# Kernel tuning notes

Measured on AMD Instinct MI355X. Metric: run time of the kernel, lower is better.

Reference implementation:

```python
import jax, jax.numpy as jnp
import numpy as np

N, L, H, D, NCLS = 8192, 1024, 512, 256, 2


def setup_inputs() -> dict:
    key = jax.random.key(0)
    ks = jax.random.split(key, 11)
    s = 0.02  # xavier-ish init scale
    return {
        "x": jax.random.normal(ks[0], (N, L), jnp.float32),
        "W_fc": jax.random.normal(ks[1], (L, H), jnp.float32) * s,
        "b_fc": jnp.zeros((H,), jnp.float32),
        "W_a": jax.random.normal(ks[2], (H, D), jnp.float32) * s,
        "b_a": jnp.zeros((D,), jnp.float32),
        "W_b": jax.random.normal(ks[3], (H, D), jnp.float32) * s,
        "b_b": jnp.zeros((D,), jnp.float32),
        "W_c": jax.random.normal(ks[4], (D, 1), jnp.float32) * s,
        "b_c": jnp.zeros((1,), jnp.float32),
        "W_cls": jax.random.normal(ks[5], (H, NCLS), jnp.float32) * s,
        "b_cls": jnp.zeros((NCLS,), jnp.float32),
    }


def reference(x, W_fc, b_fc, W_a, b_a, W_b, b_b, W_c, b_c, W_cls, b_cls):
    n = x.shape[0]
    # fc: Linear + ReLU (dropout p=0, eval)
    h = jax.nn.relu(x @ W_fc + b_fc)                      # [N, 512]
    # gated attention net (Attn_Net_Gated, n_classes=1)
    a = jnp.tanh(h @ W_a + b_a)                           # [N, 256]
    b = jax.nn.sigmoid(h @ W_b + b_b)                     # [N, 256]
    scores = ((a * b) @ W_c + b_c)[:, 0]                  # [N] diagonal scores
    # A_raw: the original's wasteful CxNxN diagonal matrix (C=1)
    idx = jnp.arange(n)
    A_raw = jnp.zeros((1, n, n), x.dtype).at[0, idx, idx].set(scores)
    # bag_forward: softmax over all N*N entries (N^2 - N zeros off-diagonal),
    # then M = (A @ h).sum(dim=1). Closed form, numerically stable:
    m = jnp.maximum(jnp.max(scores), jnp.zeros((), x.dtype))
    e = jnp.exp(scores - m)                               # diag exp terms
    e0 = jnp.exp(-m)                                      # off-diag exp(0 - m)
    Z = jnp.sum(e) + (n * n - n) * e0
    s = e / Z                                             # softmaxed diagonal
    # row_i @ h = s_i*h_i + (1/Z)*sum_{j!=i} h_j ; sum over i:
    M = s @ h + ((n - 1) * e0 / Z) * jnp.sum(h, axis=0)   # [512]
    logits = M @ W_cls + b_cls                            # [2]
    return (logits[None, :], A_raw)
```

## Files before the change

### kernel.cpp

```cpp
#include <hip/hip_runtime.h>
#include <stdint.h>

#define NROWS 8192
#define LDIM  1024
#define HDIM  512

typedef __attribute__((ext_vector_type(8))) short short8;
typedef __attribute__((ext_vector_type(4))) float f32x4;
typedef __attribute__((ext_vector_type(4))) unsigned int u32x4;

typedef __attribute__((address_space(3))) unsigned int lds_uint;
typedef const __attribute__((address_space(1))) unsigned int glob_uint;

#define Z_K1_START 0L
#define ZB_K1      3968
#define Z_G1_START 8126464L
#define ZB_G1      2560
#define Z_G2_START 13369344L
#define ZB_G2      1408
#define Z_RW_START 16252928L
#define ZB_RW      256
#define Z_END      16777215L

__device__ __forceinline__ void llds16(const void* g, void* l) {
  __builtin_amdgcn_global_load_lds((glob_uint*)g, (lds_uint*)l, 16, 0, 0);
}

__device__ __forceinline__ unsigned short f2bf(float f) {
  union { float f; unsigned int u; } c; c.f = f;
  unsigned int u = c.u;
  unsigned int r = (u + 0x7fffu + ((u >> 16) & 1u)) >> 16;
  return (unsigned short)r;
}

__device__ __forceinline__ unsigned int pkbf(float a, float b) {
  union { float f; unsigned int u; } ca, cb; ca.f = a; cb.f = b;
  return ((ca.u + 0x8000u) >> 16) | ((cb.u + 0x8000u) & 0xffff0000u);
}

__device__ __forceinline__ float bfbits2f(unsigned int hi16) {
  union { unsigned int u; float f; } c; c.u = hi16;
  return c.f;
}

__device__ __forceinline__ void zero_duty(float* __restrict__ out, long zstart, int zblk, int tid) {
  u32x4* out16 = (u32x4*)(out + 4);
  long c0 = zstart + (long)zblk * 2048;
  long c1 = c0 + 2048 < Z_END ? c0 + 2048 : Z_END;
  u32x4 z = {0u, 0u, 0u, 0u};
  for (long i = c0 + tid; i < c1; i += 256) out16[i] = z;
}

__global__ __launch_bounds__(256) void prep_kernel(const float* __restrict__ Wfc,
                                                   const float* __restrict__ Wa,
                                                   const float* __restrict__ Wb,
                                                   unsigned short* __restrict__ WfcT,
                                                   unsigned short* __restrict__ WabT,
                                                   float* __restrict__ out) {
  __shared__ float tile[32][33];
  const int bid = blockIdx.x;
  const int tid = threadIdx.x;
  if (bid < ZB_K1) {
    zero_duty(out, Z_K1_START, bid, tid);
    if (bid == 0 && tid == 0) {
      out[2] = 0.f; out[3] = 0.f;
      out[67108864] = 0.f; out[67108865] = 0.f;
    }
    return;
  }
  int tt = bid - ZB_K1;
  const float* src; unsigned short* dst; int srcn, dstk, k0, n0, mode;
  if (tt < 512) {
    src = Wfc; dst = WfcT; srcn = 512; dstk = 1024; mode = 0;
    k0 = (tt >> 4) * 32; n0 = (tt & 15) * 32;
  } else if (tt < 640) {
    int t2 = tt - 512;
    src = Wa; dst = WabT; srcn = 256; dstk = 512; mode = 1;
    k0 = (t2 >> 3) * 32; n0 = (t2 & 7) * 32;
  } else {
    int t2 = tt - 640;
    src = Wb; dst = WabT; srcn = 256; dstk = 512; mode = 2;
    k0 = (t2 >> 3) * 32; n0 = (t2 & 7) * 32;
  }
  int r = tid >> 3, c4 = (tid & 7) * 4;
  float4 v = *(const float4*)(src + (long)(k0 + r) * srcn + n0 + c4);
  tile[r][c4 + 0] = v.x; tile[r][c4 + 1] = v.y; tile[r][c4 + 2] = v.z; tile[r][c4 + 3] = v.w;
  __syncthreads();
  union { unsigned short s[4]; uint2 u; } o;
#pragma unroll
  for (int j = 0; j < 4; ++j) o.s[j] = f2bf(tile[c4 + j][r]);
  int n = n0 + r;
  long crow = (mode == 0) ? (long)n
                          : (long)(((n >> 4) << 5) + (n & 15) + (mode == 2 ? 16 : 0));
  *(uint2*)(dst + crow * dstk + k0 + c4) = o.u;
}

__global__ __launch_bounds__(256) void gemm1_kernel(const float* __restrict__ X,
                                                    const unsigned short* __restrict__ Bt,
                                                    const float* __restrict__ bias,
                                                    unsigned short* __restrict__ out,
                                                    float* __restrict__ zout) {
  constexpr int K = LDIM, nk = K / 32;
  __shared__ float sA[2][64 * 32];
  __shared__ unsigned short sB[2][128 * 32];
  const int tid = threadIdx.x;
  if ((int)blockIdx.x >= 512) {
    zero_duty(zout, Z_G1_START, (int)blockIdx.x - 512, tid);
    return;
  }
  const int lane = tid & 63;
  const int wv = tid >> 6;
  const int wm = wv >> 1, wn = wv & 1;
  const int bm = blockIdx.x >> 2, bn = blockIdx.x & 3;
  const int row0 = bm * 64, col0 = bn * 128;

  f32x4 acc[2][4] = {};

  auto stage = [&](int buf, int kt) {
#pragma unroll
    for (int r = 0; r < 2; ++r) {
      int c = r * 256 + tid;
      int ar = c >> 3, as = (c & 7) ^ (ar & 7);
      llds16(X + (long)(row0 + ar) * K + kt * 32 + as * 4,
             (float*)&sA[buf][(r * 256 + wv * 64) * 4]);
      int br = c >> 2, bs = (c & 3) ^ ((br >> 1) & 3);
      llds16(Bt + (long)(col0 + br) * K + kt * 32 + bs * 8,
             (unsigned short*)&sB[buf][(r * 256 + wv * 64) * 8]);
    }
  };

  stage(0, 0);
  __syncthreads();

  for (int kt = 0; kt < nk; ++kt) {
    int cur = kt & 1;
    if (kt + 1 < nk) stage(cur ^ 1, kt + 1);
    const float* bA = sA[cur];
    const unsigned short* bB = sB[cur];
    short8 af[2], bfr[4];
#pragma unroll
    for (int fm = 0; fm < 2; ++fm) {
      int r = wm * 32 + fm * 16 + (lane & 15);
      int g = r & 7;
      int s0 = (lane >> 4) * 2;
      float4 f0 = *(const float4*)&bA[r * 32 + ((s0)     ^ g) * 4];
      float4 f1 = *(const float4*)&bA[r * 32 + ((s0 + 1) ^ g) * 4];
      union { unsigned int u[4]; short8 s8; } o;
      o.u[0] = pkbf(f0.x, f0.y); o.u[1] = pkbf(f0.z, f0.w);
      o.u[2] = pkbf(f1.x, f1.y); o.u[3] = pkbf(f1.z, f1.w);
      af[fm] = o.s8;
    }
#pragma unroll
    for (int fn = 0; fn < 4; ++fn) {
      int rb = wn * 64 + fn * 16 + (lane & 15);
      int sb = (lane >> 4) ^ ((rb >> 1) & 3);
      bfr[fn] = *(const short8*)&bB[rb * 32 + sb * 8];
    }
#pragma unroll
    for (int fm = 0; fm < 2; ++fm)
#pragma unroll
      for (int fn = 0; fn < 4; ++fn)
        acc[fm][fn] = __builtin_amdgcn_mfma_f32_16x16x32_bf16(af[fm], bfr[fn], acc[fm][fn], 0, 0, 0);
    __syncthreads();
  }

  const float* bias_ = bias;
#pragma unroll
  for (int fm = 0; fm < 2; ++fm)
#pragma unroll
    for (int fn = 0; fn < 4; ++fn)
#pragma unroll
      for (int i = 0; i < 4; ++i) {
        int row = row0 + wm * 32 + fm * 16 + (lane >> 4) * 4 + i;
        int col = col0 + wn * 64 + fn * 16 + (lane & 15);
        float v = acc[fm][fn][i] + bias_[col];
        v = v > 0.f ? v : 0.f;
        out[(long)row * HDIM + col] = f2bf(v);
      }
}

__global__ __launch_bounds__(256) void gemm2_kernel(const unsigned short* __restrict__ A,
                                                    const unsigned short* __restrict__ Bt,
                                                    const float* __restrict__ ba_,
                                                    const float* __restrict__ bb_,
                                                    const float* __restrict__ Wc_,
                                                    float* __restrict__ spart,
                                                    float* __restrict__ zout) {
  constexpr int K = HDIM, nk = K / 32;
  __shared__ unsigned short sA[2][64 * 32];
  __shared__ unsigned short sB[2][128 * 32];
  const int tid = threadIdx.x;
  if ((int)blockIdx.x >= 512) {
    zero_duty(zout, Z_G2_START, (int)blockIdx.x - 512, tid);
    return;
  }
  const int lane = tid & 63;
  const int wv = tid >> 6;
  const int wm = wv >> 1, wn = wv & 1;
  const int bm = blockIdx.x >> 2, bn = blockIdx.x & 3;
  const int row0 = bm * 64, col0 = bn * 128;

  f32x4 acc[2][4] = {};

  auto stage = [&](int buf, int kt) {
    {
      int ar = tid >> 2, as = (tid & 3) ^ ((ar >> 1) & 3);
      llds16(A + (long)(row0 + ar) * K + kt * 32 + as * 8,
             (unsigned short*)&sA[buf][(wv * 64) * 8]);
    }
#pragma unroll
    for (int r = 0; r < 2; ++r) {
      int c = r * 256 + tid;
      int br = c >> 2, bs = (c & 3) ^ ((br >> 1) & 3);
      llds16(Bt + (long)(col0 + br) * K + kt * 32 + bs * 8,
             (unsigned short*)&sB[buf][(r * 256 + wv * 64) * 8]);
    }
  };

  stage(0, 0);
  __syncthreads();

  for (int kt = 0; kt < nk; ++kt) {
    int cur = kt & 1;
    if (kt + 1 < nk) stage(cur ^ 1, kt + 1);
    const unsigned short* bA = sA[cur];
    const unsigned short* bB = sB[cur];
    short8 af[2], bfr[4];
#pragma unroll
    for (int fm = 0; fm < 2; ++fm) {
      int r = wm * 32 + fm * 16 + (lane & 15);
      int s = (lane >> 4) ^ ((r >> 1) & 3);
      af[fm] = *(const short8*)&bA[r * 32 + s * 8];
    }
#pragma unroll
    for (int fn = 0; fn < 4; ++fn) {
      int rb = wn * 64 + fn * 16 + (lane & 15);
      int sb = (lane >> 4) ^ ((rb >> 1) & 3);
      bfr[fn] = *(const short8*)&bB[rb * 32 + sb * 8];
    }
#pragma unroll
    for (int fm = 0; fm < 2; ++fm)
#pragma unroll
      for (int fn = 0; fn < 4; ++fn)
        acc[fm][fn] = __builtin_amdgcn_mfma_f32_16x16x32_bf16(af[fm], bfr[fn], acc[fm][fn], 0, 0, 0);
    __syncthreads();
  }

#pragma unroll
  for (int g = 0; g < 2; ++g) {
    const int colg = col0 + wn * 64 + g * 32;
    const int d0 = (colg >> 5) * 16 + (lane & 15);
    float wc = Wc_[d0], av = ba_[d0], bv = bb_[d0];
    float* sp = spart + (long)(colg >> 5) * NROWS;
#pragma unroll
    for (int fm = 0; fm < 2; ++fm)
#pragma unroll
      for (int i = 0; i < 4; ++i) {
        float aa = acc[fm][g * 2 + 0][i] + av;
        float bbv = acc[fm][g * 2 + 1][i] + bv;
        float v = tanhf(aa) * (1.f / (1.f + __expf(-bbv))) * wc;
#pragma unroll
        for (int off = 1; off < 16; off <<= 1) v += __shfl_xor(v, off);
        if ((lane & 15) == 0)
          sp[row0 + wm * 32 + fm * 16 + (lane >> 4) * 4 + i] = v;
      }
  }
}

__global__ __launch_bounds__(256) void redwsum_kernel(const float* __restrict__ spart,
                                                      const float* __restrict__ bc,
                                                      const unsigned short* __restrict__ h,
                                                      float* __restrict__ part,
                                                      float* __restrict__ out) {
  const int b = blockIdx.x;
  const int t = threadIdx.x;
  if (b >= 64) {
    zero_duty(out, Z_RW_START, b - 64, t);
    return;
  }
  __shared__ float sc[NROWS];
  __shared__ float red[256];
  __shared__ float warr[128];
  const float bcv = bc[0];
  float lmax = -1e30f;
  for (int k = t; k < NROWS; k += 256) {
    float s = bcv;
#pragma unroll
    for (int q = 0; q < 16; ++q) s += spart[q * NROWS + k];
    sc[k] = s;
    lmax = fmaxf(lmax, s);
  }
  red[t] = lmax; __syncthreads();
  for (int s = 128; s; s >>= 1) { if (t < s) red[t] = fmaxf(red[t], red[t + s]); __syncthreads(); }
  float m = fmaxf(red[0], 0.f);
  __syncthreads();
  float lsum = 0.f;
  for (int k = t; k < NROWS; k += 256) lsum += __expf(sc[k] - m);
  red[t] = lsum; __syncthreads();
  for (int s = 128; s; s >>= 1) { if (t < s) red[t] += red[t + s]; __syncthreads(); }
  float e0 = __expf(-m);
  float Z = red[0] + 67100672.0f * e0;
  float c0w = 8191.0f * e0 / Z;
  if (t < 128) warr[t] = __expf(sc[b * 128 + t] - m) / Z + c0w;
  __syncthreads();
  float a0 = 0.f, a1 = 0.f;
  for (int i = 0; i < 128; ++i) {
    float wi = warr[i];
    unsigned int hv = *(const unsigned int*)&h[(long)(b * 128 + i) * 512 + t * 2];
    a0 += wi * bfbits2f(hv << 16);
    a1 += wi * bfbits2f(hv & 0xffff0000u);
  }
  part[b * 512 + t * 2] = a0;
  part[b * 512 + t * 2 + 1] = a1;
}

__global__ __launch_bounds__(512) void final_kernel(const float* __restrict__ part,
                                                    const float* __restrict__ spart,
                                                    const float* __restrict__ bc,
                                                    const float* __restrict__ Wcls,
                                                    const float* __restrict__ bcls,
                                                    float* __restrict__ out) {
  const int t = threadIdx.x;
  if (blockIdx.x > 0) {
    if (t < 256) {
      int row = (blockIdx.x - 1) * 256 + t;
      float s = bc[0];
#pragma unroll
      for (int q = 0; q < 16; ++q) s += spart[q * NROWS + row];
      out[2 + 8193L * row] = s;
    }
    return;
  }
  __shared__ float Msh[512];
  float s = 0.f;
  for (int b = 0; b < 64; ++b) s += part[b * 512 + t];
  Msh[t] = s;
  __syncthreads();
  if (t < 64) {
    float p0 = 0.f, p1 = 0.f;
    for (int j = t; j < 512; j += 64) { p0 += Msh[j] * Wcls[j * 2]; p1 += Msh[j] * Wcls[j * 2 + 1]; }
#pragma unroll
    for (int off = 32; off; off >>= 1) { p0 += __shfl_down(p0, off); p1 += __shfl_down(p1, off); }
    if (t == 0) { out[0] = p0 + bcls[0]; out[1] = p1 + bcls[1]; }
  }
}

extern "C" void kernel_launch(void* const* d_in, const int* in_sizes, int n_in,
                              void* d_out, int out_size, void* d_ws, size_t ws_size,
                              hipStream_t stream) {
  const float* x    = (const float*)d_in[0];
  const float* Wfc  = (const float*)d_in[1];
  const float* bfc  = (const float*)d_in[2];
  const float* Wa   = (const float*)d_in[3];
  const float* ba   = (const float*)d_in[4];
  const float* Wb   = (const float*)d_in[5];
  const float* bb   = (const float*)d_in[6];
  const float* Wc   = (const float*)d_in[7];
  const float* bc   = (const float*)d_in[8];
  const float* Wcls = (const float*)d_in[9];
  const float* bcls = (const float*)d_in[10];
  float* out = (float*)d_out;
  char* ws = (char*)d_ws;

  unsigned short* WfcT  = (unsigned short*)(ws + 0);
  unsigned short* WabT  = (unsigned short*)(ws + 1048576);
  unsigned short* hbuf  = (unsigned short*)(ws + 1572864);
  float*          spart = (float*)(ws + 9961472);
  float*          part  = (float*)(ws + 10485760);

  prep_kernel<<<ZB_K1 + 768, 256, 0, stream>>>(Wfc, Wa, Wb, WfcT, WabT, out);
  gemm1_kernel<<<512 + ZB_G1, 256, 0, stream>>>(x, WfcT, bfc, hbuf, out);
  gemm2_kernel<<<512 + ZB_G2, 256, 0, stream>>>(hbuf, WabT, ba, bb, Wc, spart, out);
  redwsum_kernel<<<64 + ZB_RW, 256, 0, stream>>>(spart, bc, hbuf, part, out);
  final_kernel<<<33, 512, 0, stream>>>(part, spart, bc, Wcls, bcls, out);
}
```

Measured before the change: 123.8 us.

## Convert X to bf16 during staging, remap GEMM blocks, rebalance zeroing across kernels

GEMM1 now loads X through registers and converts it to bf16 before writing LDS, rather than staging fp32 in LDS and converting per fragment. The conversion and LDS store are placed after the MFMAs so they overlap the next tile's load, and LDS for A is halved. Both GEMMs use a block index remap that groups row tiles for L2 locality and drop the XOR swizzle, which may bring back LDS bank conflicts. The zero-fill of the big output is removed from the prep kernel and spread over the GEMM and reduction kernels.

```diff
diff --git a/kernel.cpp b/kernel.cpp
--- a/kernel.cpp
+++ b/kernel.cpp
@@ -12,14 +12,12 @@
 typedef __attribute__((address_space(3))) unsigned int lds_uint;
 typedef const __attribute__((address_space(1))) unsigned int glob_uint;
 
-#define Z_K1_START 0L
-#define ZB_K1      3968
-#define Z_G1_START 8126464L
-#define ZB_G1      2560
-#define Z_G2_START 13369344L
-#define ZB_G2      1408
-#define Z_RW_START 16252928L
-#define ZB_RW      256
+#define Z_G1_START 0L
+#define ZB_G1      4800
+#define Z_G2_START 9830400L
+#define ZB_G2      2240
+#define Z_RW_START 14417920L
+#define ZB_RW      1152
 #define Z_END      16777215L
 
 __device__ __forceinline__ void llds16(const void* g, void* l) {
@@ -55,20 +53,10 @@
                                                    const float* __restrict__ Wa,
                                                    const float* __restrict__ Wb,
                                                    unsigned short* __restrict__ WfcT,
-                                                   unsigned short* __restrict__ WabT,
-                                                   float* __restrict__ out) {
+                                                   unsigned short* __restrict__ WabT) {
   __shared__ float tile[32][33];
-  const int bid = blockIdx.x;
   const int tid = threadIdx.x;
-  if (bid < ZB_K1) {
-    zero_duty(out, Z_K1_START, bid, tid);
-    if (bid == 0 && tid == 0) {
-      out[2] = 0.f; out[3] = 0.f;
-      out[67108864] = 0.f; out[67108865] = 0.f;
-    }
-    return;
-  }
-  int tt = bid - ZB_K1;
+  int tt = blockIdx.x;
   const float* src; unsigned short* dst; int srcn, dstk, k0, n0, mode;
   if (tt < 512) {
     src = Wfc; dst = WfcT; srcn = 512; dstk = 1024; mode = 0;
@@ -101,70 +89,83 @@
                                                     unsigned short* __restrict__ out,
                                                     float* __restrict__ zout) {
   constexpr int K = LDIM, nk = K / 32;
-  __shared__ float sA[2][64 * 32];
+  __shared__ unsigned short sA[2][64 * 32];
   __shared__ unsigned short sB[2][128 * 32];
   const int tid = threadIdx.x;
   if ((int)blockIdx.x >= 512) {
-    zero_duty(zout, Z_G1_START, (int)blockIdx.x - 512, tid);
+    int zblk = (int)blockIdx.x - 512;
+    zero_duty(zout, Z_G1_START, zblk, tid);
+    if (zblk == 0 && tid == 0) {
+      zout[3] = 0.f;
+      zout[67108864] = 0.f;
+    }
     return;
   }
+  const int gid = blockIdx.x;
+  const int bm = (gid & 7) * 16 + ((gid >> 3) & 15);
+  const int bn = gid >> 7;
   const int lane = tid & 63;
   const int wv = tid >> 6;
   const int wm = wv >> 1, wn = wv & 1;
-  const int bm = blockIdx.x >> 2, bn = blockIdx.x & 3;
   const int row0 = bm * 64, col0 = bn * 128;
+  const int arow = tid >> 2, acol = (tid & 3) * 8;
+  const float* xsrc = X + (long)(row0 + arow) * K + acol;
+  unsigned short* aw0 = &sA[0][arow * 32 + acol];
+  unsigned short* aw1 = &sA[1][arow * 32 + acol];
 
   f32x4 acc[2][4] = {};
 
-  auto stage = [&](int buf, int kt) {
+  auto stageB = [&](int buf, int kt) {
 #pragma unroll
     for (int r = 0; r < 2; ++r) {
       int c = r * 256 + tid;
-      int ar = c >> 3, as = (c & 7) ^ (ar & 7);
-      llds16(X + (long)(row0 + ar) * K + kt * 32 + as * 4,
-             (float*)&sA[buf][(r * 256 + wv * 64) * 4]);
-      int br = c >> 2, bs = (c & 3) ^ ((br >> 1) & 3);
-      llds16(Bt + (long)(col0 + br) * K + kt * 32 + bs * 8,
+      llds16(Bt + (long)(col0 + (c >> 2)) * K + kt * 32 + (c & 3) * 8,
              (unsigned short*)&sB[buf][(r * 256 + wv * 64) * 8]);
     }
   };
 
-  stage(0, 0);
+  {
+    float4 f0 = *(const float4*)(xsrc);
+    float4 f1 = *(const float4*)(xsrc + 4);
+    stageB(0, 0);
+    union { unsigned int u[4]; uint4 v; } oa;
+    oa.u[0] = pkbf(f0.x, f0.y); oa.u[1] = pkbf(f0.z, f0.w);
+    oa.u[2] = pkbf(f1.x, f1.y); oa.u[3] = pkbf(f1.z, f1.w);
+    *(uint4*)aw0 = oa.v;
+  }
   __syncthreads();
 
   for (int kt = 0; kt < nk; ++kt) {
     int cur = kt & 1;
-    if (kt + 1 < nk) stage(cur ^ 1, kt + 1);
-    const float* bA = sA[cur];
+    float4 f0, f1;
+    if (kt + 1 < nk) {
+      f0 = *(const float4*)(xsrc + (kt + 1) * 32);
+      f1 = *(const float4*)(xsrc + (kt + 1) * 32 + 4);
+      stageB(cur ^ 1, kt + 1);
+    }
+    const unsigned short* bA = sA[cur];
     const unsigned short* bB = sB[cur];
     short8 af[2], bfr[4];
 #pragma unroll
-    for (int fm = 0; fm < 2; ++fm) {
-      int r = wm * 32 + fm * 16 + (lane & 15);
-      int g = r & 7;
-      int s0 = (lane >> 4) * 2;
-      float4 f0 = *(const float4*)&bA[r * 32 + ((s0)     ^ g) * 4];
-      float4 f1 = *(const float4*)&bA[r * 32 + ((s0 + 1) ^ g) * 4];
-      union { unsigned int u[4]; short8 s8; } o;
-      o.u[0] = pkbf(f0.x, f0.y); o.u[1] = pkbf(f0.z, f0.w);
-      o.u[2] = pkbf(f1.x, f1.y); o.u[3] = pkbf(f1.z, f1.w);
-      af[fm] = o.s8;
-    }
-#pragma unroll
-    for (int fn = 0; fn < 4; ++fn) {
-      int rb = wn * 64 + fn * 16 + (lane & 15);
-      int sb = (lane >> 4) ^ ((rb >> 1) & 3);
-      bfr[fn] = *(const short8*)&bB[rb * 32 + sb * 8];
-    }
+    for (int fm = 0; fm < 2; ++fm)
+      af[fm] = *(const short8*)&bA[(wm * 32 + fm * 16 + (lane & 15)) * 32 + (lane >> 4) * 8];
+#pragma unroll
+    for (int fn = 0; fn < 4; ++fn)
+      bfr[fn] = *(const short8*)&bB[(wn * 64 + fn * 16 + (lane & 15)) * 32 + (lane >> 4) * 8];
 #pragma unroll
     for (int fm = 0; fm < 2; ++fm)
 #pragma unroll
       for (int fn = 0; fn < 4; ++fn)
         acc[fm][fn] = __builtin_amdgcn_mfma_f32_16x16x32_bf16(af[fm], bfr[fn], acc[fm][fn], 0, 0, 0);
+    if (kt + 1 < nk) {
+      union { unsigned int u[4]; uint4 v; } oa;
+      oa.u[0] = pkbf(f0.x, f0.y); oa.u[1] = pkbf(f0.z, f0.w);
+      oa.u[2] = pkbf(f1.x, f1.y); oa.u[3] = pkbf(f1.z, f1.w);
+      *(uint4*)(cur ? aw0 : aw1) = oa.v;
+    }
     __syncthreads();
   }
 
-  const float* bias_ = bias;
 #pragma unroll
   for (int fm = 0; fm < 2; ++fm)
 #pragma unroll
@@ -173,7 +174,7 @@
       for (int i = 0; i < 4; ++i) {
         int row = row0 + wm * 32 + fm * 16 + (lane >> 4) * 4 + i;
         int col = col0 + wn * 64 + fn * 16 + (lane & 15);
-        float v = acc[fm][fn][i] + bias_[col];
+        float v = acc[fm][fn][i] + bias[col];
         v = v > 0.f ? v : 0.f;
         out[(long)row * HDIM + col] = f2bf(v);
       }
@@ -194,25 +195,23 @@
     zero_duty(zout, Z_G2_START, (int)blockIdx.x - 512, tid);
     return;
   }
+  const int gid = blockIdx.x;
+  const int bm = (gid & 7) * 16 + ((gid >> 3) & 15);
+  const int bn = gid >> 7;
   const int lane = tid & 63;
   const int wv = tid >> 6;
   const int wm = wv >> 1, wn = wv & 1;
-  const int bm = blockIdx.x >> 2, bn = blockIdx.x & 3;
   const int row0 = bm * 64, col0 = bn * 128;
+  const int arow = tid >> 2, acb = (tid & 3) * 8;
 
   f32x4 acc[2][4] = {};
 
   auto stage = [&](int buf, int kt) {
-    {
-      int ar = tid >> 2, as = (tid & 3) ^ ((ar >> 1) & 3);
-      llds16(A + (long)(row0 + ar) * K + kt * 32 + as * 8,
-             (unsigned short*)&sA[buf][(wv * 64) * 8]);
-    }
+    llds16(A + (long)(row0 + arow) * K + kt * 32 + acb, (unsigned short*)&sA[buf][(wv * 64) * 8]);
 #pragma unroll
     for (int r = 0; r < 2; ++r) {
       int c = r * 256 + tid;
-      int br = c >> 2, bs = (c & 3) ^ ((br >> 1) & 3);
-      llds16(Bt + (long)(col0 + br) * K + kt * 32 + bs * 8,
+      llds16(Bt + (long)(col0 + (c >> 2)) * K + kt * 32 + (c & 3) * 8,
              (unsigned short*)&sB[buf][(r * 256 + wv * 64) * 8]);
     }
   };
@@ -227,17 +226,11 @@
     const unsigned short* bB = sB[cur];
     short8 af[2], bfr[4];
 #pragma unroll
-    for (int fm = 0; fm < 2; ++fm) {
-      int r = wm * 32 + fm * 16 + (lane & 15);
-      int s = (lane >> 4) ^ ((r >> 1) & 3);
-      af[fm] = *(const short8*)&bA[r * 32 + s * 8];
-    }
-#pragma unroll
-    for (int fn = 0; fn < 4; ++fn) {
-      int rb = wn * 64 + fn * 16 + (lane & 15);
-      int sb = (lane >> 4) ^ ((rb >> 1) & 3);
-      bfr[fn] = *(const short8*)&bB[rb * 32 + sb * 8];
-    }
+    for (int fm = 0; fm < 2; ++fm)
+      af[fm] = *(const short8*)&bA[(wm * 32 + fm * 16 + (lane & 15)) * 32 + (lane >> 4) * 8];
+#pragma unroll
+    for (int fn = 0; fn < 4; ++fn)
+      bfr[fn] = *(const short8*)&bB[(wn * 64 + fn * 16 + (lane & 15)) * 32 + (lane >> 4) * 8];
 #pragma unroll
     for (int fm = 0; fm < 2; ++fm)
 #pragma unroll
@@ -368,7 +361,7 @@
   float*          spart = (float*)(ws + 9961472);
   float*          part  = (float*)(ws + 10485760);
 
-  prep_kernel<<<ZB_K1 + 768, 256, 0, stream>>>(Wfc, Wa, Wb, WfcT, WabT, out);
+  prep_kernel<<<768, 256, 0, stream>>>(Wfc, Wa, Wb, WfcT, WabT);
   gemm1_kernel<<<512 + ZB_G1, 256, 0, stream>>>(x, WfcT, bfc, hbuf, out);
   gemm2_kernel<<<512 + ZB_G2, 256, 0, stream>>>(hbuf, WabT, ba, bb, Wc, spart, out);
   redwsum_kernel<<<64 + ZB_RW, 256, 0, stream>>>(spart, bc, hbuf, part, out);
```

Result: slower. 126.6 us (+2.3%).
